# Kernel tuning notes

Measured on AMD Instinct MI355X. Metric: run time of the kernel, lower is better.

The kernel has to match this reference:

```python
import jax, jax.numpy as jnp
import numpy as np
from jax import lax

P = 192      # patches per frame
PS = 7       # patch size
GH, GW = 16, 16  # grid cells
DS = 4       # encoder downsize factor
CH = 128     # feature channels
KS, PAD = 7, 3  # harris avg-pool kernel / padding


def _encoder(x, w, b):
    # stand-in encoder: conv(1->CH, k=7, stride=DS, pad=3) + relu
    y = lax.conv_general_dilated(x, w, (DS, DS), [(PAD, PAD), (PAD, PAD)],
                                 dimension_numbers=('NCHW', 'OIHW', 'NCHW'))
    return jax.nn.relu(y + b[None, :, None, None])


def _harris(frame):
    b, n, c, h, w = frame.shape
    f = frame.reshape(b * n, c, h, w)
    dx = jnp.pad(f[..., 1:] - f[..., :-1], ((0, 0), (0, 0), (0, 0), (0, 1)), mode='reflect')
    dy = jnp.pad(f[..., 1:, :] - f[..., :-1, :], ((0, 0), (0, 0), (0, 1), (0, 0)), mode='reflect')
    def avg(x):
        s = lax.reduce_window(x, 0.0, lax.add, (1, 1, KS, KS), (1, 1, 1, 1),
                              [(0, 0), (0, 0), (PAD, PAD), (PAD, PAD)])
        return s / (KS * KS)  # count_include_pad=True like torch avg_pool2d
    Ixx, Iyy, Ixy = avg(dx * dx), avg(dy * dy), avg(dx * dy)
    return (Ixx * Iyy - Ixy * Ixy) / (Ixx + Iyy + 1e-8)


def _best_coords(g):
    bn, _, h, w = g.shape
    ph = -(-h // GH); pw = -(-w // GW)
    g = jnp.pad(g, ((0, 0), (0, 0), (0, ph * GH - h), (0, pw * GW - w)))
    g = g.reshape(bn, GH, ph, GW, pw).transpose(0, 1, 3, 2, 4).reshape(bn, GH, GW, ph * pw)
    idx = jnp.argmax(g, axis=-1)
    vals = jnp.max(g, axis=-1)
    yg = idx // pw + (ph * jnp.arange(GH))[None, :, None]
    xg = idx % pw + (pw * jnp.arange(GW))[None, None, :]
    _, top = lax.top_k(vals.reshape(bn, -1), P)
    yb = jnp.take_along_axis(yg.reshape(bn, -1), top, 1)
    xb = jnp.take_along_axis(xg.reshape(bn, -1), top, 1)
    return jnp.stack([xb, yb], -1).astype(jnp.float32)  # (bn, P, 2)


def _bilinear(img, xs, ys):
    # img (c,h,w); xs,ys (N,) pixel coords; zero padding, align_corners=False
    c, h, w = img.shape
    x0 = jnp.floor(xs); y0 = jnp.floor(ys)
    wx = xs - x0; wy = ys - y0
    x0i = x0.astype(jnp.int32); y0i = y0.astype(jnp.int32)
    out = jnp.zeros((c, xs.shape[0]), img.dtype)
    for dxi, dyi, wt in ((0, 0, (1 - wx) * (1 - wy)), (1, 0, wx * (1 - wy)),
                         (0, 1, (1 - wx) * wy), (1, 1, wx * wy)):
        xi = x0i + dxi; yi = y0i + dyi
        m = ((xi >= 0) & (xi < w) & (yi >= 0) & (yi < h)).astype(img.dtype)
        v = img[:, jnp.clip(yi, 0, h - 1), jnp.clip(xi, 0, w - 1)]
        out = out + v * (wt * m)[None, :]
    return out


def _patches(coords, fmap, cmap):
    bn, c, h, w = fmap.shape
    coords = coords / DS
    r = jnp.arange(-(PS // 2), PS // 2 + 1, dtype=jnp.float32)
    dy, dx = jnp.meshgrid(r, r, indexing='ij')
    off = jnp.stack([dx, dy], -1)                       # (PS,PS,2)
    cp = coords[:, :, None, None, :] + off[None, None]  # (bn,P,PS,PS,2)
    xp = cp[..., 0].reshape(bn, -1); yp = cp[..., 1].reshape(bn, -1)
    pf = jax.vmap(_bilinear)(fmap, xp, yp)              # (bn,c,P*PS*PS)
    pf = pf.reshape(bn, c, P, PS * PS).transpose(0, 2, 1, 3)
    pc = jax.vmap(_bilinear)(cmap, coords[..., 0], coords[..., 1])  # (bn,c,P)
    pc = pc.transpose(0, 2, 1)
    return pf, pc


def setup_inputs() -> dict:
    key = jax.random.key(0)
    k1, k2, k3 = jax.random.split(key, 3)
    frame = jax.random.uniform(k1, (4, 2, 1, 480, 640), dtype=jnp.float32)
    w_f = jax.random.normal(k2, (CH, 1, KS, KS), dtype=jnp.float32) * 0.1
    w_c = jax.random.normal(k3, (CH, 1, KS, KS), dtype=jnp.float32) * 0.1
    b_f = jnp.zeros((CH,), jnp.float32)
    b_c = jnp.zeros((CH,), jnp.float32)
    return {"frame": frame, "w_f": w_f, "b_f": b_f, "w_c": w_c, "b_c": b_c}


def reference(frame, w_f, b_f, w_c, b_c):
    b, n, c, h, w = frame.shape
    f2 = frame.reshape(b * n, c, h, w)
    fmap = _encoder(f2, w_f, b_f)
    imap = _encoder(f2, w_c, b_c)
    g = _harris(frame)
    coords = _best_coords(g)
    patches_f, patches_c = _patches(coords, fmap, imap)
    return coords, patches_f, patches_c, fmap
```

## Files before the change

### kernel.cpp

```cpp
#include <hip/hip_runtime.h>
#include <hip/hip_bf16.h>
#include <math.h>

#define BN    8
#define H     480
#define W     640
#define CH    128
#define OH    120
#define OW    160
#define P     192
#define PS    7
#define GH    16
#define GW    16
#define PH    30
#define PW    40

__global__ __launch_bounds__(256) void conv_enc(
    const float* __restrict__ f,
    const float* __restrict__ wf, const float* __restrict__ bf,
    float* __restrict__ fmap)
{
    __shared__ float s[35][132];

    int blk = blockIdx.x;
    int tx = blk % 5;
    int ty = (blk / 5) % 15;
    int b  = blk / 75;
    int ox0 = tx * 32, oy0 = ty * 8;
    int c0 = blockIdx.y * 64;
    int tid = threadIdx.x;
    int ix_base = 4 * ox0 - 3, iy_base = 4 * oy0 - 3;
    const float* fb = f + (size_t)b * H * W;

    for (int i = tid; i < 35 * 132; i += 256) {
        int r = i / 132, c = i % 132;
        int gy = iy_base + r, gx = ix_base + c;
        s[r][c] = (gy >= 0 && gy < H && gx >= 0 && gx < W)
                ? fb[(size_t)gy * W + gx] : 0.0f;
    }
    __syncthreads();

    int oxl = tid & 31, oyl = tid >> 5;
    float in[49];
    #pragma unroll
    for (int ky = 0; ky < 7; ky++) {
        const float4 a  = *(const float4*)&s[4 * oyl + ky][4 * oxl];
        const float4 b4 = *(const float4*)&s[4 * oyl + ky][4 * oxl + 4];
        in[ky * 7 + 0] = a.x;  in[ky * 7 + 1] = a.y;
        in[ky * 7 + 2] = a.z;  in[ky * 7 + 3] = a.w;
        in[ky * 7 + 4] = b4.x; in[ky * 7 + 5] = b4.y;
        in[ky * 7 + 6] = b4.z;
    }

    int ox = ox0 + oxl, oy = oy0 + oyl;
    size_t obase = (size_t)b * CH * (OH * OW) + (size_t)oy * OW + ox;
    for (int c = c0; c < c0 + 64; c++) {
        const float* wfc = wf + c * 49;
        float af = bf[c];
        #pragma unroll
        for (int k = 0; k < 49; k++) af = fmaf(wfc[k], in[k], af);
        fmap[obase + (size_t)c * (OH * OW)] = fmaxf(af, 0.0f);
    }
}

__global__ __launch_bounds__(256) void harris_cell(
    const float* __restrict__ f, float* __restrict__ cval, int* __restrict__ cidx)
{
    __shared__ float sf[37][48];
    __shared__ float dxx[36][48], dyy[36][48], dxy[36][48];
    __shared__ float sv[256];
    __shared__ int   si[256];

    int cell = blockIdx.x;
    int b  = cell >> 8;
    int ci = cell & 255;
    int gh = ci >> 4, gw = ci & 15;
    int cy0 = gh * PH, cx0 = gw * PW;
    const float* fb = f + (size_t)b * H * W;
    int tid = threadIdx.x;

    for (int i = tid; i < 37 * 47; i += 256) {
        int r = i / 47, c = i % 47;
        int y = min(max(cy0 - 3 + r, 0), H - 1);
        int x = min(max(cx0 - 3 + c, 0), W - 1);
        sf[r][c] = fb[(size_t)y * W + x];
    }
    __syncthreads();

    for (int i = tid; i < 36 * 46; i += 256) {
        int r = i / 46, c = i % 46;
        int y = cy0 - 3 + r;
        int x = cx0 - 3 + c;
        float vxx = 0.0f, vyy = 0.0f, vxy = 0.0f;
        if (y >= 0 && y < H && x >= 0 && x < W) {
            int xa = (x == W - 1) ? (x - 2) : x;
            int ya = (y == H - 1) ? (y - 2) : y;
            int lx = xa - (cx0 - 3);
            int ly = ya - (cy0 - 3);
            float dxv = sf[r][lx + 1] - sf[r][lx];
            float dyv = sf[ly + 1][c] - sf[ly][c];
            vxx = dxv * dxv;
            vyy = dyv * dyv;
            vxy = dxv * dyv;
        }
        dxx[r][c] = vxx; dyy[r][c] = vyy; dxy[r][c] = vxy;
    }
    __syncthreads();

    float best = -INFINITY;
    int   bidx = 0x7fffffff;
    for (int i = tid; i < PH * PW; i += 256) {
        int iy = i / PW, ix = i % PW;
        float Sxx = 0.0f, Syy = 0.0f, Sxy = 0.0f;
        #pragma unroll
        for (int ky = 0; ky < 7; ky++) {
            #pragma unroll
            for (int kx = 0; kx < 7; kx++) {
                Sxx += dxx[iy + ky][ix + kx];
                Syy += dyy[iy + ky][ix + kx];
                Sxy += dxy[iy + ky][ix + kx];
            }
        }
        float Ixx = Sxx / 49.0f;
        float Iyy = Syy / 49.0f;
        float Ixy = Sxy / 49.0f;
        float resp = (Ixx * Iyy - Ixy * Ixy) / (Ixx + Iyy + 1e-8f);
        if (resp > best) { best = resp; bidx = i; }
    }

    sv[tid] = best;
    si[tid] = bidx;
    __syncthreads();
    for (int s = 128; s > 0; s >>= 1) {
        if (tid < s) {
            float ov = sv[tid + s];
            int   oi = si[tid + s];
            if (ov > sv[tid] || (ov == sv[tid] && oi < si[tid])) {
                sv[tid] = ov; si[tid] = oi;
            }
        }
        __syncthreads();
    }
    if (tid == 0) { cval[cell] = sv[0]; cidx[cell] = si[0]; }
}

__global__ __launch_bounds__(256) void topk_coords(
    const float* __restrict__ cval, const int* __restrict__ cidx,
    float* __restrict__ coords)
{
    int b = blockIdx.x;
    int j = threadIdx.x;
    __shared__ float v[256];
    v[j] = cval[b * 256 + j];
    __syncthreads();
    float vj = v[j];
    int rank = 0;
    for (int k = 0; k < 256; k++) {
        float vk = v[k];
        rank += (vk > vj) || (vk == vj && k < j);
    }
    if (rank < P) {
        int ii = cidx[b * 256 + j];
        int gh = j >> 4, gw = j & 15;
        int y = ii / PW + gh * PH;
        int x = ii % PW + gw * PW;
        coords[((size_t)b * P + rank) * 2 + 0] = (float)x;
        coords[((size_t)b * P + rank) * 2 + 1] = (float)y;
    }
}

__global__ __launch_bounds__(256) void patches_kern(
    const float* __restrict__ coords,
    const float* __restrict__ fmap,
    const float* __restrict__ frame,
    const float* __restrict__ wc, const float* __restrict__ bc,
    float* __restrict__ pf, float* __restrict__ pc)
{
    __shared__ float sfm[CH][64];
    __shared__ float sf2[14][16];
    __shared__ float vq[CH][5];

    int bp = blockIdx.x;
    int b = bp / P;
    float cx = coords[(size_t)bp * 2 + 0] * 0.25f;
    float cy = coords[(size_t)bp * 2 + 1] * 0.25f;
    int tid = threadIdx.x;

    int X0 = (int)floorf(cx), Y0 = (int)floorf(cy);
    float wx = cx - (float)X0, wy = cy - (float)Y0;
    float w00 = (1.0f - wx) * (1.0f - wy);
    float w10 = wx * (1.0f - wy);
    float w01 = (1.0f - wx) * wy;
    float w11 = wx * wy;

    const float* fm = fmap + (size_t)b * CH * (OH * OW);
    for (int i = tid; i < CH * 64; i += 256) {
        int ch = i >> 6;
        int off = i & 63;
        int r = off >> 3, c = off & 7;
        int gy = Y0 - 3 + r, gx = X0 - 3 + c;
        sfm[ch][off] = (gy >= 0 && gy < OH && gx >= 0 && gx < OW)
                     ? fm[(size_t)ch * (OH * OW) + gy * OW + gx] : 0.0f;
    }

    int ix0 = 4 * X0 - 3, iy0 = 4 * Y0 - 3;
    const float* frb = frame + (size_t)b * H * W;
    for (int i = tid; i < 14 * 14; i += 256) {
        int r = i / 14, c = i % 14;
        int y = iy0 + r, x = ix0 + c;
        sf2[r][c] = (y >= 0 && y < H && x >= 0 && x < W)
                  ? frb[(size_t)y * W + x] : 0.0f;
    }
    __syncthreads();

    size_t pfbase = (size_t)bp * CH * 49;
    for (int idx = tid; idx < CH * 49; idx += 256) {
        int c = idx / 49;
        int k = idx - c * 49;
        int ky = k / 7, kx = k - ky * 7;
        int o = ky * 8 + kx;
        float acc = w00 * sfm[c][o]
                  + w10 * sfm[c][o + 1]
                  + w01 * sfm[c][o + 8]
                  + w11 * sfm[c][o + 9];
        pf[pfbase + idx] = acc;
    }

    for (int idx = tid; idx < 512; idx += 256) {
        int q = idx & 3;
        int c = idx >> 2;
        int qx = q & 1, qy = q >> 1;
        const float* wcc = wc + c * 49;
        float acc = bc[c];
        #pragma unroll
        for (int ky = 0; ky < 7; ky++) {
            #pragma unroll
            for (int kx = 0; kx < 7; kx++)
                acc = fmaf(wcc[ky * 7 + kx], sf2[4 * qy + ky][4 * qx + kx], acc);
        }
        vq[c][q] = fmaxf(acc, 0.0f);
    }
    __syncthreads();

    float m00 = (X0 >= 0 && X0 < OW && Y0 >= 0 && Y0 < OH) ? 1.0f : 0.0f;
    float m10 = (X0 + 1 >= 0 && X0 + 1 < OW && Y0 >= 0 && Y0 < OH) ? 1.0f : 0.0f;
    float m01 = (X0 >= 0 && X0 < OW && Y0 + 1 >= 0 && Y0 + 1 < OH) ? 1.0f : 0.0f;
    float m11 = (X0 + 1 >= 0 && X0 + 1 < OW && Y0 + 1 >= 0 && Y0 + 1 < OH) ? 1.0f : 0.0f;
    if (tid < CH) {
        float acc = w00 * m00 * vq[tid][0] + w10 * m10 * vq[tid][1]
                  + w01 * m01 * vq[tid][2] + w11 * m11 * vq[tid][3];
        pc[(size_t)bp * CH + tid] = acc;
    }
}

extern "C" void kernel_launch(void* const* d_in, const int* in_sizes, int n_in,
                              void* d_out, int out_size, void* d_ws, size_t ws_size,
                              hipStream_t stream)
{
    const float* frame = (const float*)d_in[0];
    const float* w_f   = (const float*)d_in[1];
    const float* b_f   = (const float*)d_in[2];
    const float* w_c   = (const float*)d_in[3];
    const float* b_c   = (const float*)d_in[4];

    float* out = (float*)d_out;
    const size_t coords_sz = (size_t)BN * P * 2;
    const size_t pf_sz     = (size_t)BN * P * CH * 49;
    const size_t pc_sz     = (size_t)BN * P * CH;
    float* coords = out;
    float* pf     = out + coords_sz;
    float* pc     = out + coords_sz + pf_sz;
    float* fmap   = out + coords_sz + pf_sz + pc_sz;

    float* cval = (float*)d_ws;
    int*   cidx = (int*)(cval + BN * 256);

    dim3 cg(600, 2);
    conv_enc<<<cg, 256, 0, stream>>>(frame, w_f, b_f, fmap);

    harris_cell<<<BN * 256, 256, 0, stream>>>(frame, cval, cidx);

    topk_coords<<<BN, 256, 0, stream>>>(cval, cidx, coords);

    patches_kern<<<BN * P, 256, 0, stream>>>(
        coords, fmap, frame, w_c, b_c, pf, pc);
}
```

Measured before the change: 290.5 us.

## Split conv channels across more blocks, unroll 4 channels, reuse Harris window rows

The conv encoder now gives each block 32 output channels instead of 64, doubling the grid to 600x4. Each thread computes 4 channels at once so every input value it loads feeds four FMA chains, which adds instruction-level parallelism. The Harris box filter now assigns one column and 6 consecutive output rows to each of 200 threads. Each shared-memory row of the window is read once and added into every output it covers, so shared loads are reused across rows. In exchange, the input tile is loaded twice as many times and Harris uses more registers, leaving 56 threads idle.

```diff
diff --git a/kernel.cpp b/kernel.cpp
--- a/kernel.cpp
+++ b/kernel.cpp
@@ -27,7 +27,7 @@
     int ty = (blk / 5) % 15;
     int b  = blk / 75;
     int ox0 = tx * 32, oy0 = ty * 8;
-    int c0 = blockIdx.y * 64;
+    int c0 = blockIdx.y * 32;
     int tid = threadIdx.x;
     int ix_base = 4 * ox0 - 3, iy_base = 4 * oy0 - 3;
     const float* fb = f + (size_t)b * H * W;
@@ -54,12 +54,25 @@
 
     int ox = ox0 + oxl, oy = oy0 + oyl;
     size_t obase = (size_t)b * CH * (OH * OW) + (size_t)oy * OW + ox;
-    for (int c = c0; c < c0 + 64; c++) {
-        const float* wfc = wf + c * 49;
-        float af = bf[c];
+    for (int cc = 0; cc < 32; cc += 4) {
+        int c = c0 + cc;
+        const float* w0 = wf + c * 49;
+        const float* w1 = w0 + 49;
+        const float* w2 = w0 + 98;
+        const float* w3 = w0 + 147;
+        float a0 = bf[c], a1 = bf[c + 1], a2 = bf[c + 2], a3 = bf[c + 3];
         #pragma unroll
-        for (int k = 0; k < 49; k++) af = fmaf(wfc[k], in[k], af);
-        fmap[obase + (size_t)c * (OH * OW)] = fmaxf(af, 0.0f);
+        for (int k = 0; k < 49; k++) {
+            float x = in[k];
+            a0 = fmaf(w0[k], x, a0);
+            a1 = fmaf(w1[k], x, a1);
+            a2 = fmaf(w2[k], x, a2);
+            a3 = fmaf(w3[k], x, a3);
+        }
+        fmap[obase + (size_t)(c    ) * (OH * OW)] = fmaxf(a0, 0.0f);
+        fmap[obase + (size_t)(c + 1) * (OH * OW)] = fmaxf(a1, 0.0f);
+        fmap[obase + (size_t)(c + 2) * (OH * OW)] = fmaxf(a2, 0.0f);
+        fmap[obase + (size_t)(c + 3) * (OH * OW)] = fmaxf(a3, 0.0f);
     }
 }
 
@@ -109,23 +122,43 @@
 
     float best = -INFINITY;
     int   bidx = 0x7fffffff;
-    for (int i = tid; i < PH * PW; i += 256) {
-        int iy = i / PW, ix = i % PW;
-        float Sxx = 0.0f, Syy = 0.0f, Sxy = 0.0f;
+    if (tid < 200) {
+        int col = tid % 40;
+        int grp = tid / 40;
+        int iy0 = grp * 6;
+        float axx[6] = {0,0,0,0,0,0};
+        float ayy[6] = {0,0,0,0,0,0};
+        float axy[6] = {0,0,0,0,0,0};
         #pragma unroll
-        for (int ky = 0; ky < 7; ky++) {
+        for (int r = 0; r < 12; r++) {
+            float vxx[7], vyy[7], vxy[7];
             #pragma unroll
             for (int kx = 0; kx < 7; kx++) {
-                Sxx += dxx[iy + ky][ix + kx];
-                Syy += dyy[iy + ky][ix + kx];
-                Sxy += dxy[iy + ky][ix + kx];
+                vxx[kx] = dxx[iy0 + r][col + kx];
+                vyy[kx] = dyy[iy0 + r][col + kx];
+                vxy[kx] = dxy[iy0 + r][col + kx];
             }
-        }
-        float Ixx = Sxx / 49.0f;
-        float Iyy = Syy / 49.0f;
-        float Ixy = Sxy / 49.0f;
-        float resp = (Ixx * Iyy - Ixy * Ixy) / (Ixx + Iyy + 1e-8f);
-        if (resp > best) { best = resp; bidx = i; }
+            #pragma unroll
+            for (int p = 0; p < 6; p++) {
+                if (r - p >= 0 && r - p <= 6) {
+                    #pragma unroll
+                    for (int kx = 0; kx < 7; kx++) {
+                        axx[p] += vxx[kx];
+                        ayy[p] += vyy[kx];
+                        axy[p] += vxy[kx];
+                    }
+                }
+            }
+        }
+        #pragma unroll
+        for (int p = 0; p < 6; p++) {
+            float Ixx = axx[p] / 49.0f;
+            float Iyy = ayy[p] / 49.0f;
+            float Ixy = axy[p] / 49.0f;
+            float resp = (Ixx * Iyy - Ixy * Ixy) / (Ixx + Iyy + 1e-8f);
+            int idx = (iy0 + p) * PW + col;
+            if (resp > best) { best = resp; bidx = idx; }
+        }
     }
 
     sv[tid] = best;
@@ -275,7 +308,7 @@
     float* cval = (float*)d_ws;
     int*   cidx = (int*)(cval + BN * 256);
 
-    dim3 cg(600, 2);
+    dim3 cg(600, 4);
     conv_enc<<<cg, 256, 0, stream>>>(frame, w_f, b_f, fmap);
 
     harris_cell<<<BN * 256, 256, 0, stream>>>(frame, cval, cidx);
```

Result: slower. 462.6 us (+59.2%).
